# Optimization experiments

Hardware: AMD Instinct MI355X
Metric: run time of the kernel (lower is better)

The kernel has to match this reference:

```python
import jax, jax.numpy as jnp
import numpy as np

B, F, V, D = 16384, 26, 100000, 64
H1, H2 = 512, 256
IN_DIM = F * D + F * (F - 1) // 2  # 1664 + 325 = 1989
# upper-triangle (i<j) pair indices in row-major order == itertools.combinations order
IU, JU = np.triu_indices(F, k=1)


def setup_inputs() -> dict:
    key = jax.random.key(0)
    ks = jax.random.split(key, 9)
    idx = jax.random.randint(ks[0], (B, F), 0, V)
    tables = jax.random.normal(ks[1], (F, V, D), dtype=jnp.float32) * 0.01
    W1 = jax.random.normal(ks[2], (IN_DIM, H1), dtype=jnp.float32) * (IN_DIM ** -0.5)
    b1 = jnp.zeros((H1,), jnp.float32)
    W2 = jax.random.normal(ks[3], (H1, H2), dtype=jnp.float32) * (H1 ** -0.5)
    b2 = jnp.zeros((H2,), jnp.float32)
    W3 = jax.random.normal(ks[4], (H2, 1), dtype=jnp.float32) * (H2 ** -0.5)
    b3 = jnp.zeros((1,), jnp.float32)
    return {"idx": idx, "tables": tables, "W1": W1, "b1": b1,
            "W2": W2, "b2": b2, "W3": W3, "b3": b3}


def reference(idx, tables, W1, b1, W2, b2, W3, b3):
    # embedding lookup: tables[f, idx[b, f]] -> [B, F, D]
    emb = tables[jnp.arange(F)[None, :], idx]
    # fused dot-interaction: batched Gram matrix + triangular gather
    gram = jnp.einsum('bfd,bgd->bfg', emb, emb)  # [B, F, F]
    inter = gram[:, IU, JU]                      # [B, F*(F-1)/2]
    joint = jnp.concatenate([emb.reshape(B, F * D), inter], axis=1)
    h = jax.nn.relu(joint @ W1 + b1)
    h = jax.nn.relu(h @ W2 + b2)
    return (h @ W3 + b3).squeeze(-1)  # [B] logits
```

## Files before the change

kernel.cpp:

```cpp
#include <hip/hip_runtime.h>

#define B_SZ   16384
#define F_N    26
#define V_N    100000
#define D_N    64
#define H1_N   512
#define H2_N   256
#define IN_DIM 1989
#define KPAD   2048

typedef _Float16 half8_t __attribute__((ext_vector_type(8)));
typedef _Float16 half4_t __attribute__((ext_vector_type(4)));
typedef float    floatx4 __attribute__((ext_vector_type(4)));

#define MFMA16(a, b, c) __builtin_amdgcn_mfma_f32_16x16x32_f16((a), (b), (c), 0, 0, 0)

__device__ __forceinline__ void load_lds16(const void* g, void* l) {
    __builtin_amdgcn_global_load_lds(
        (const __attribute__((address_space(1))) unsigned int*)g,
        (__attribute__((address_space(3))) unsigned int*)l,
        16, 0, 0);
}

__global__ __launch_bounds__(256) void prep_w(const float* __restrict__ W,
                                              _Float16* __restrict__ WT,
                                              int K, int N, int Kpad) {
    int t = blockIdx.x * 256 + threadIdx.x;
    if (t >= N * Kpad) return;
    int k = t / N;
    int n = t - k * N;
    WT[(size_t)n * Kpad + k] = (k < K) ? (_Float16)W[(size_t)k * N + n] : (_Float16)0.f;
}

#define EMB_STRIDE 72
#define EMB_PER_SAMPLE (32 * EMB_STRIDE)

__global__ __launch_bounds__(256) void gather_interact(
        const int* __restrict__ idx,
        const float* __restrict__ tables,
        _Float16* __restrict__ joint) {
    __shared__ __align__(16) _Float16 embh[4 * EMB_PER_SAMPLE];
    __shared__ int sidx[4 * F_N];
    const int tid = threadIdx.x;
    const int b0  = blockIdx.x * 4;

    if (tid < 4 * F_N) sidx[tid] = idx[(size_t)b0 * F_N + tid];

    for (int z = tid; z < 4 * 6 * 16; z += 256) {
        int s = z / 96, rem = z % 96;
        int f = F_N + rem / 16, d4 = (rem % 16) * 4;
        half4_t zz; zz[0] = 0; zz[1] = 0; zz[2] = 0; zz[3] = 0;
        *(half4_t*)(embh + s * EMB_PER_SAMPLE + f * EMB_STRIDE + d4) = zz;
    }
    __syncthreads();

    float4 v[7];
    #pragma unroll
    for (int i = 0; i < 7; ++i) {
        int c = tid + i * 256;
        if (c < 4 * F_N * 16) {
            int s = c / 416, rem = c - s * 416;
            int f = rem >> 4, d4 = (rem & 15) * 4;
            v[i] = *(const float4*)(tables +
                     ((size_t)f * V_N + sidx[s * F_N + f]) * D_N + d4);
        }
    }
    #pragma unroll
    for (int i = 0; i < 7; ++i) {
        int c = tid + i * 256;
        if (c < 4 * F_N * 16) {
            int s = c / 416, rem = c - s * 416;
            int f = rem >> 4, d4 = (rem & 15) * 4;
            half4_t h;
            h[0] = (_Float16)v[i].x; h[1] = (_Float16)v[i].y;
            h[2] = (_Float16)v[i].z; h[3] = (_Float16)v[i].w;
            *(half4_t*)(embh + s * EMB_PER_SAMPLE + f * EMB_STRIDE + d4) = h;
            *(half4_t*)(joint + (size_t)(b0 + s) * KPAD + f * D_N + d4) = h;
        }
    }
    for (int q = tid; q < 4 * (KPAD - IN_DIM); q += 256) {
        int s = q / (KPAD - IN_DIM), p = q % (KPAD - IN_DIM);
        joint[(size_t)(b0 + s) * KPAD + IN_DIM + p] = (_Float16)0.f;
    }
    __syncthreads();

    const int wave = tid >> 6, lane = tid & 63;
    const _Float16* eb = embh + wave * EMB_PER_SAMPLE;
    const int fr = lane & 15;
    const int fk = (lane >> 4) * 8;
    floatx4 a00 = {0.f, 0.f, 0.f, 0.f};
    floatx4 a01 = {0.f, 0.f, 0.f, 0.f};
    floatx4 a11 = {0.f, 0.f, 0.f, 0.f};
    #pragma unroll
    for (int k0 = 0; k0 < 64; k0 += 32) {
        half8_t f0 = *(const half8_t*)(eb + fr * EMB_STRIDE + k0 + fk);
        half8_t f1 = *(const half8_t*)(eb + (16 + fr) * EMB_STRIDE + k0 + fk);
        a00 = MFMA16(f0, f0, a00);
        a01 = MFMA16(f0, f1, a01);
        a11 = MFMA16(f1, f1, a11);
    }
    _Float16* jrow = joint + (size_t)(b0 + wave) * KPAD + F_N * D_N;
    #pragma unroll
    for (int r = 0; r < 4; ++r) {
        int mb = (lane >> 4) * 4 + r;
        {
            int m = mb, n = fr;
            if (m < n) jrow[(m * (51 - m)) / 2 + n - m - 1] = (_Float16)a00[r];
        }
        {
            int m = mb, n = 16 + fr;
            if (n < F_N) jrow[(m * (51 - m)) / 2 + n - m - 1] = (_Float16)a01[r];
        }
        {
            int m = 16 + mb, n = 16 + fr;
            if (m < n && n < F_N) jrow[(m * (51 - m)) / 2 + n - m - 1] = (_Float16)a11[r];
        }
    }
}

__global__ __launch_bounds__(256) void gemm_bt(
        const _Float16* __restrict__ A, int lda,
        const _Float16* __restrict__ Bt, int ldb,
        const float* __restrict__ bias,
        _Float16* __restrict__ C, int ldc,
        int K, int nblocks) {
    __shared__ __align__(16) _Float16 As[2][128 * 32];
    __shared__ __align__(16) _Float16 Bs[2][128 * 32];
    const int tid  = threadIdx.x;
    const int wave = tid >> 6;
    const int lane = tid & 63;
    int bid = blockIdx.x;
    if ((gridDim.x & 7) == 0) {
        const int cpx = gridDim.x >> 3;
        bid = (bid & 7) * cpx + (bid >> 3);
    }
    const int bm = bid / nblocks;
    const int bn = bid % nblocks;
    const int m0 = bm * 128, n0 = bn * 128;

    const int c0 = tid, c1 = tid + 256;
    const _Float16* ag0 = A  + (size_t)(m0 + (c0 >> 2)) * lda + (c0 & 3) * 8;
    const _Float16* ag1 = A  + (size_t)(m0 + (c1 >> 2)) * lda + (c1 & 3) * 8;
    const _Float16* bg0 = Bt + (size_t)(n0 + (c0 >> 2)) * ldb + (c0 & 3) * 8;
    const _Float16* bg1 = Bt + (size_t)(n0 + (c1 >> 2)) * ldb + (c1 & 3) * 8;

    floatx4 acc[4][4];
    #pragma unroll
    for (int i = 0; i < 4; ++i)
        #pragma unroll
        for (int j = 0; j < 4; ++j) acc[i][j] = (floatx4){0.f, 0.f, 0.f, 0.f};

    const int wm = (wave >> 1) * 64;
    const int wn = (wave & 1) * 64;
    const int fr = lane & 15;
    const int fk = (lane >> 4) * 8;

    auto stage = [&](int buf, int k0) {
        char* ab = (char*)As + buf * 8192;
        char* bb = (char*)Bs + buf * 8192;
        load_lds16(ag0 + k0, ab + wave * 1024);
        load_lds16(ag1 + k0, ab + 4096 + wave * 1024);
        load_lds16(bg0 + k0, bb + wave * 1024);
        load_lds16(bg1 + k0, bb + 4096 + wave * 1024);
    };
    auto compute = [&](int buf) {
        const _Float16* as = &As[buf][0];
        const _Float16* bs = &Bs[buf][0];
        half8_t af[4], bf[4];
        #pragma unroll
        for (int i = 0; i < 4; ++i)
            af[i] = *(const half8_t*)(as + (wm + i * 16 + fr) * 32 + fk);
        #pragma unroll
        for (int j = 0; j < 4; ++j)
            bf[j] = *(const half8_t*)(bs + (wn + j * 16 + fr) * 32 + fk);
        #pragma unroll
        for (int i = 0; i < 4; ++i)
            #pragma unroll
            for (int j = 0; j < 4; ++j)
                acc[i][j] = MFMA16(af[i], bf[j], acc[i][j]);
    };

    stage(0, 0);
    __syncthreads();
    int cur = 0;
    for (int k0 = 32; k0 < K; k0 += 32) {
        stage(cur ^ 1, k0);
        compute(cur);
        __syncthreads();
        cur ^= 1;
    }
    compute(cur);

    const int colb = n0 + wn + fr;
    const int rowb = m0 + wm + (lane >> 4) * 4;
    #pragma unroll
    for (int j = 0; j < 4; ++j) {
        const int c = colb + j * 16;
        const float bv = bias[c];
        #pragma unroll
        for (int i = 0; i < 4; ++i)
            #pragma unroll
            for (int r = 0; r < 4; ++r) {
                float v = acc[i][j][r] + bv;
                v = fmaxf(v, 0.f);
                C[(size_t)(rowb + i * 16 + r) * ldc + c] = (_Float16)v;
            }
    }
}

__global__ __launch_bounds__(256) void fused_tail(
        const _Float16* __restrict__ h1, const _Float16* __restrict__ W2T,
        const float* __restrict__ b2, const float* __restrict__ W3,
        const float* __restrict__ b3, float* __restrict__ out) {
    __shared__ __align__(16) _Float16 As[2][64 * 32];
    __shared__ __align__(16) _Float16 Bs[2][256 * 32];
    __shared__ float red[4][64];
    const int tid  = threadIdx.x;
    const int wave = tid >> 6;
    const int lane = tid & 63;
    const int m0 = blockIdx.x * 64;

    const _Float16* ag  = h1  + (size_t)(m0 + (tid >> 2)) * H1_N + (tid & 3) * 8;
    const _Float16* bg0 = W2T + (size_t)(tid >> 2) * H1_N + (tid & 3) * 8;

    floatx4 acc[4][4];
    #pragma unroll
    for (int i = 0; i < 4; ++i)
        #pragma unroll
        for (int j = 0; j < 4; ++j) acc[i][j] = (floatx4){0.f, 0.f, 0.f, 0.f};

    const int wn = wave * 64;
    const int fr = lane & 15;
    const int fk = (lane >> 4) * 8;

    auto stage = [&](int buf, int k0) {
        char* ab = (char*)As + buf * 4096;
        char* bb = (char*)Bs + buf * 16384;
        load_lds16(ag + k0, ab + wave * 1024);
        #pragma unroll
        for (int i = 0; i < 4; ++i)
            load_lds16(bg0 + (size_t)i * 64 * H1_N + k0,
                       bb + i * 4096 + wave * 1024);
    };
    auto compute = [&](int buf) {
        const _Float16* as = &As[buf][0];
        const _Float16* bs = &Bs[buf][0];
        half8_t af[4], bf[4];
        #pragma unroll
        for (int i = 0; i < 4; ++i)
            af[i] = *(const half8_t*)(as + (i * 16 + fr) * 32 + fk);
        #pragma unroll
        for (int j = 0; j < 4; ++j)
            bf[j] = *(const half8_t*)(bs + (wn + j * 16 + fr) * 32 + fk);
        #pragma unroll
        for (int i = 0; i < 4; ++i)
            #pragma unroll
            for (int j = 0; j < 4; ++j)
                acc[i][j] = MFMA16(af[i], bf[j], acc[i][j]);
    };

    stage(0, 0);
    __syncthreads();
    int cur = 0;
    for (int k0 = 32; k0 < H1_N; k0 += 32) {
        stage(cur ^ 1, k0);
        compute(cur);
        __syncthreads();
        cur ^= 1;
    }
    compute(cur);

    float b2v[4], w3v[4];
    #pragma unroll
    for (int j = 0; j < 4; ++j) {
        const int c = wn + j * 16 + fr;
        b2v[j] = b2[c];
        w3v[j] = W3[c];
    }
    #pragma unroll
    for (int i = 0; i < 4; ++i)
        #pragma unroll
        for (int r = 0; r < 4; ++r) {
            float p = 0.f;
            #pragma unroll
            for (int j = 0; j < 4; ++j) {
                float h = acc[i][j][r] + b2v[j];
                h = fmaxf(h, 0.f);
                p += h * w3v[j];
            }
            p += __shfl_xor(p, 1, 16);
            p += __shfl_xor(p, 2, 16);
            p += __shfl_xor(p, 4, 16);
            p += __shfl_xor(p, 8, 16);
            if (fr == 0)
                red[wave][i * 16 + (lane >> 4) * 4 + r] = p;
        }
    __syncthreads();
    if (tid < 64) {
        float s = red[0][tid] + red[1][tid] + red[2][tid] + red[3][tid] + b3[0];
        out[m0 + tid] = s;
    }
}

extern "C" void kernel_launch(void* const* d_in, const int* in_sizes, int n_in,
                              void* d_out, int out_size, void* d_ws, size_t ws_size,
                              hipStream_t stream) {
    const int*   idx    = (const int*)d_in[0];
    const float* tables = (const float*)d_in[1];
    const float* W1     = (const float*)d_in[2];
    const float* b1     = (const float*)d_in[3];
    const float* W2     = (const float*)d_in[4];
    const float* b2     = (const float*)d_in[5];
    const float* W3     = (const float*)d_in[6];
    const float* b3     = (const float*)d_in[7];
    float* out = (float*)d_out;

    char* ws = (char*)d_ws;
    _Float16* joint = (_Float16*)(ws);
    _Float16* W1T   = (_Float16*)(ws + 67108864);
    _Float16* h1    = (_Float16*)(ws + 69206016);
    _Float16* W2T   = (_Float16*)(ws + 85983232);

    prep_w<<<(H1_N * KPAD + 255) / 256, 256, 0, stream>>>(W1, W1T, IN_DIM, H1_N, KPAD);
    prep_w<<<(H2_N * H1_N + 255) / 256, 256, 0, stream>>>(W2, W2T, H1_N, H2_N, H1_N);
    gather_interact<<<B_SZ / 4, 256, 0, stream>>>(idx, tables, joint);
    gemm_bt<<<(B_SZ / 128) * (H1_N / 128), 256, 0, stream>>>(
        joint, KPAD, W1T, KPAD, b1, h1, H1_N, KPAD, H1_N / 128);
    fused_tail<<<B_SZ / 64, 256, 0, stream>>>(h1, W2T, b2, W3, b3, out);
}
```

Measured before the change: 824.8 us.

## Fold weight prep into gather kernel and triple-buffer GEMM K-loop

Removes the two prep_w launches by doing the W1/W2 transpose-to-fp16 inside the gather_interact blocks (4096 blocks × 256 threads covers 512×2048 exactly). The first-layer GEMM moves from double to triple buffering in LDS, with explicit vmcnt waits and a single barrier per step so global loads run two stages ahead. This cuts launch overhead and exposes more memory latency to overlap. The cost is more LDS per block, which may reduce occupancy, and reliance on hand-counted vmcnt(4) matching the stage's load count.

```diff
diff --git a/kernel.cpp b/kernel.cpp
--- a/kernel.cpp
+++ b/kernel.cpp
@@ -22,27 +22,32 @@
         16, 0, 0);
 }
 
-__global__ __launch_bounds__(256) void prep_w(const float* __restrict__ W,
-                                              _Float16* __restrict__ WT,
-                                              int K, int N, int Kpad) {
-    int t = blockIdx.x * 256 + threadIdx.x;
-    if (t >= N * Kpad) return;
-    int k = t / N;
-    int n = t - k * N;
-    WT[(size_t)n * Kpad + k] = (k < K) ? (_Float16)W[(size_t)k * N + n] : (_Float16)0.f;
-}
-
 #define EMB_STRIDE 72
 #define EMB_PER_SAMPLE (32 * EMB_STRIDE)
 
 __global__ __launch_bounds__(256) void gather_interact(
         const int* __restrict__ idx,
         const float* __restrict__ tables,
-        _Float16* __restrict__ joint) {
+        _Float16* __restrict__ joint,
+        const float* __restrict__ W1,
+        const float* __restrict__ W2,
+        _Float16* __restrict__ W1T,
+        _Float16* __restrict__ W2T) {
     __shared__ __align__(16) _Float16 embh[4 * EMB_PER_SAMPLE];
     __shared__ int sidx[4 * F_N];
     const int tid = threadIdx.x;
     const int b0  = blockIdx.x * 4;
+
+    {
+        int t = blockIdx.x * 256 + tid;
+        int k = t >> 9, n = t & 511;
+        W1T[(size_t)n * KPAD + k] =
+            (k < IN_DIM) ? (_Float16)W1[(size_t)k * H1_N + n] : (_Float16)0.f;
+        if (blockIdx.x < 512) {
+            int k2 = t >> 8, n2 = t & 255;
+            W2T[(size_t)n2 * H1_N + k2] = (_Float16)W2[(size_t)k2 * H2_N + n2];
+        }
+    }
 
     if (tid < 4 * F_N) sidx[tid] = idx[(size_t)b0 * F_N + tid];
 
@@ -124,8 +129,8 @@
         const float* __restrict__ bias,
         _Float16* __restrict__ C, int ldc,
         int K, int nblocks) {
-    __shared__ __align__(16) _Float16 As[2][128 * 32];
-    __shared__ __align__(16) _Float16 Bs[2][128 * 32];
+    __shared__ __align__(16) _Float16 As[3][128 * 32];
+    __shared__ __align__(16) _Float16 Bs[3][128 * 32];
     const int tid  = threadIdx.x;
     const int wave = tid >> 6;
     const int lane = tid & 63;
@@ -180,16 +185,19 @@
                 acc[i][j] = MFMA16(af[i], bf[j], acc[i][j]);
     };
 
+    const int nsteps = K >> 5;
     stage(0, 0);
-    __syncthreads();
-    int cur = 0;
-    for (int k0 = 32; k0 < K; k0 += 32) {
-        stage(cur ^ 1, k0);
-        compute(cur);
-        __syncthreads();
-        cur ^= 1;
-    }
-    compute(cur);
+    stage(1, 32);
+    int i = 0;
+    for (; i < nsteps - 1; ++i) {
+        asm volatile("s_waitcnt vmcnt(4)" ::: "memory");
+        __builtin_amdgcn_s_barrier();
+        if (i + 2 < nsteps) stage((i + 2) % 3, (i + 2) * 32);
+        compute(i % 3);
+    }
+    asm volatile("s_waitcnt vmcnt(0)" ::: "memory");
+    __builtin_amdgcn_s_barrier();
+    compute(i % 3);
 
     const int colb = n0 + wn + fr;
     const int rowb = m0 + wm + (lane >> 4) * 4;
@@ -198,12 +206,12 @@
         const int c = colb + j * 16;
         const float bv = bias[c];
         #pragma unroll
-        for (int i = 0; i < 4; ++i)
+        for (int i2 = 0; i2 < 4; ++i2)
             #pragma unroll
             for (int r = 0; r < 4; ++r) {
-                float v = acc[i][j][r] + bv;
+                float v = acc[i2][j][r] + bv;
                 v = fmaxf(v, 0.f);
-                C[(size_t)(rowb + i * 16 + r) * ldc + c] = (_Float16)v;
+                C[(size_t)(rowb + i2 * 16 + r) * ldc + c] = (_Float16)v;
             }
     }
 }
@@ -321,9 +329,8 @@
     _Float16* h1    = (_Float16*)(ws + 69206016);
     _Float16* W2T   = (_Float16*)(ws + 85983232);
 
-    prep_w<<<(H1_N * KPAD + 255) / 256, 256, 0, stream>>>(W1, W1T, IN_DIM, H1_N, KPAD);
-    prep_w<<<(H2_N * H1_N + 255) / 256, 256, 0, stream>>>(W2, W2T, H1_N, H2_N, H1_N);
-    gather_interact<<<B_SZ / 4, 256, 0, stream>>>(idx, tables, joint);
+    gather_interact<<<B_SZ / 4, 256, 0, stream>>>(idx, tables, joint,
+                                                  W1, W2, W1T, W2T);
     gemm_bt<<<(B_SZ / 128) * (H1_N / 128), 256, 0, stream>>>(
         joint, KPAD, W1T, KPAD, b1, h1, H1_N, KPAD, H1_N / 128);
     fused_tail<<<B_SZ / 64, 256, 0, stream>>>(h1, W2T, b2, W3, b3, out);
```

After: 814.4 us. No clear change (-1.3%).
